# Kernel optimization log

Hardware: AMD Instinct MI355X
Metric: run time of the kernel (lower is better)

Reference implementation:

```python
import jax, jax.numpy as jnp
import numpy as np

B = 1024          # global batch
D = 512           # embedding_size
C = 100000        # num_classes (sum over 8 shards)
S = 64.0          # ArcFace scale
M = 0.5           # ArcFace additive angular margin
EPS = 1e-30


def setup_inputs() -> dict:
    key = jax.random.key(0)
    k1, k2, k3 = jax.random.split(key, 3)
    embeddings = jax.random.normal(k1, (B, D), dtype=jnp.float32)
    weight = jax.random.normal(k2, (C, D), dtype=jnp.float32)
    labels = jax.random.randint(k3, (B,), 0, C, dtype=jnp.int64)
    return {"embeddings": embeddings, "weight": weight, "labels": labels}


def reference(embeddings, weight, labels):
    # normalize(embeddings), normalize(weight) -> cosine logits
    ne = embeddings * jax.lax.rsqrt(jnp.sum(embeddings * embeddings, axis=1, keepdims=True))
    nw = weight * jax.lax.rsqrt(jnp.sum(weight * weight, axis=1, keepdims=True))
    logits = jnp.clip(jnp.einsum("bd,cd->bc", ne, nw), -1.0, 1.0)  # [B, C]

    rows = jnp.arange(B)
    target_logit = logits[rows, labels]
    # ArcFace: cos(theta + m), theta+m clipped to pi (insightface CombinedMarginLoss m2)
    theta = jnp.arccos(jnp.clip(target_logit, -1.0, 1.0))
    new_target = jnp.cos(jnp.minimum(theta + M, jnp.float32(np.pi)))
    logits = logits.at[rows, labels].set(new_target) * S

    # FusedDistCrossEntropy (single-device equivalent): stable softmax,
    # gather target prob, loss = -mean(log(clamp(p_target, 1e-30)))
    logp = jax.nn.log_softmax(logits, axis=1)
    p_target = jnp.exp(logp[rows, labels])
    loss = -jnp.mean(jnp.log(jnp.maximum(p_target, EPS)))
    return loss
```

## Files before the change

### kernel.cpp

```cpp
#include <hip/hip_runtime.h>
#include <hip/hip_bf16.h>
#include <math.h>
#include <stdint.h>

#define B_BATCH   1024
#define D_DIM     512
#define C_CLASSES 100000
#define BM        128
#define BN        128
#define BK        32
#define KITERS    (D_DIM / BK)
#define MTILES    (B_BATCH / BM)
#define NTILES    ((C_CLASSES + BN - 1) / BN)
#define LOG2E     1.44269504088896340736f
#define COSM      0.87758256189037276f
#define SINM      0.47942553860420301f
#define NEG_LOG_EPS 69.07755278982137f

typedef short bf16x8 __attribute__((ext_vector_type(8)));
typedef float f32x4  __attribute__((ext_vector_type(4)));

static __device__ __forceinline__ unsigned short f2bf(float f) {
    unsigned int u = __builtin_bit_cast(unsigned int, f);
    u += 0x7fffu + ((u >> 16) & 1u);
    return (unsigned short)(u >> 16);
}

static __device__ __forceinline__ void gld16(const unsigned short* g, unsigned short* l) {
    __builtin_amdgcn_global_load_lds(
        (const __attribute__((address_space(1))) unsigned int*)g,
        (__attribute__((address_space(3))) unsigned int*)l, 16, 0, 0);
}

__global__ __launch_bounds__(256) void norm_embed(const float* __restrict__ E,
                                                  unsigned short* __restrict__ Abf) {
    const int b = blockIdx.x;
    const int t = threadIdx.x;
    float2 v = ((const float2*)(E + (size_t)b * D_DIM))[t];
    float ss = v.x * v.x + v.y * v.y;
    #pragma unroll
    for (int off = 1; off < 64; off <<= 1) ss += __shfl_xor(ss, off);
    __shared__ float ws4[4];
    if ((t & 63) == 0) ws4[t >> 6] = ss;
    __syncthreads();
    float inv = rsqrtf(ws4[0] + ws4[1] + ws4[2] + ws4[3]);
    unsigned int packed = (unsigned int)f2bf(v.x * inv) |
                          ((unsigned int)f2bf(v.y * inv) << 16);
    ((unsigned int*)Abf)[(size_t)b * (D_DIM / 2) + t] = packed;
}

__global__ __launch_bounds__(256) void norm_weight(const float* __restrict__ W,
                                                   unsigned short* __restrict__ Wbf) {
    const int wave = threadIdx.x >> 6;
    const int lane = threadIdx.x & 63;
    const int row = blockIdx.x * 4 + wave;
    if (row >= C_CLASSES) return;
    const float4* src = (const float4*)(W + (size_t)row * D_DIM);
    float4 v0 = src[lane];
    float4 v1 = src[lane + 64];
    float ss = v0.x*v0.x + v0.y*v0.y + v0.z*v0.z + v0.w*v0.w
             + v1.x*v1.x + v1.y*v1.y + v1.z*v1.z + v1.w*v1.w;
    #pragma unroll
    for (int off = 1; off < 64; off <<= 1) ss += __shfl_xor(ss, off);
    float inv = rsqrtf(ss);
    ushort4 o0, o1;
    o0.x = f2bf(v0.x*inv); o0.y = f2bf(v0.y*inv); o0.z = f2bf(v0.z*inv); o0.w = f2bf(v0.w*inv);
    o1.x = f2bf(v1.x*inv); o1.y = f2bf(v1.y*inv); o1.z = f2bf(v1.z*inv); o1.w = f2bf(v1.w*inv);
    ushort4* dst = (ushort4*)(Wbf + (size_t)row * D_DIM);
    dst[lane] = o0;
    dst[lane + 64] = o1;
}

static __device__ __forceinline__ float epi_term(float accv, int col, int lab,
                                                 float* __restrict__ st, int srow) {
    float c = fminf(1.f, fmaxf(-1.f, accv));
    if (col >= C_CLASSES) return 0.f;
    float s = c * 64.0f;
    if (col == lab) {
        float sn = sqrtf(fmaxf(0.f, 1.f - c * c));
        float nm = c * COSM - sn * SINM;
        if (c < -COSM) nm = -1.f;
        s = nm * 64.0f;
        st[srow] = s;
    }
    return exp2f((s - 64.0f) * LOG2E);
}

__global__ __launch_bounds__(256) void gemm_cos(const unsigned short* __restrict__ Abf,
                                                const unsigned short* __restrict__ Wbf,
                                                const int* __restrict__ labels,
                                                float* __restrict__ st,
                                                float* __restrict__ partial) {
    __shared__ unsigned short As[BM * BK];
    __shared__ unsigned short Bs[BN * BK];
    __shared__ float rowSum[BM];
    __shared__ int   labs[BM];

    const int tid = threadIdx.x;
    const int m0 = blockIdx.x * BM;
    const int n0 = blockIdx.y * BN;
    if (tid < BM) { labs[tid] = labels[m0 + tid]; rowSum[tid] = 0.f; }

    const int lane = tid & 63;
    const int wave = tid >> 6;
    const int wm = wave & 1, wn = wave >> 1;
    const int l15 = lane & 15, quad = lane >> 4;

    const int rsub = lane >> 2;
    const int cg   = (lane & 3) * 8;
    const int c0 = wave * 2, c1 = wave * 2 + 1;
    const unsigned short* gA0 = Abf + (size_t)(m0 + c0 * 16 + rsub) * D_DIM + cg;
    const unsigned short* gA1 = Abf + (size_t)(m0 + c1 * 16 + rsub) * D_DIM + cg;
    const int bR0 = min(n0 + c0 * 16 + rsub, C_CLASSES - 1);
    const int bR1 = min(n0 + c1 * 16 + rsub, C_CLASSES - 1);
    const unsigned short* gB0 = Wbf + (size_t)bR0 * D_DIM + cg;
    const unsigned short* gB1 = Wbf + (size_t)bR1 * D_DIM + cg;
    unsigned short* lA0 = &As[c0 * 512];
    unsigned short* lA1 = &As[c1 * 512];
    unsigned short* lB0 = &Bs[c0 * 512];
    unsigned short* lB1 = &Bs[c1 * 512];

    const f32x4 z = (f32x4){0.f, 0.f, 0.f, 0.f};
    f32x4 a00 = z, a01 = z, a02 = z, a03 = z;
    f32x4 a10 = z, a11 = z, a12 = z, a13 = z;
    f32x4 a20 = z, a21 = z, a22 = z, a23 = z;
    f32x4 a30 = z, a31 = z, a32 = z, a33 = z;

    for (int kk = 0; kk < KITERS; ++kk) {
        __syncthreads();
        gld16(gA0, lA0); gld16(gA1, lA1);
        gld16(gB0, lB0); gld16(gB1, lB1);
        gA0 += BK; gA1 += BK; gB0 += BK; gB1 += BK;
        __syncthreads();

        const int aro = (wm * 64 + l15) * BK + quad * 8;
        const int bro = (wn * 64 + l15) * BK + quad * 8;
        bf16x8 af0 = *(const bf16x8*)&As[aro];
        bf16x8 af1 = *(const bf16x8*)&As[aro + 16 * BK];
        bf16x8 af2 = *(const bf16x8*)&As[aro + 32 * BK];
        bf16x8 af3 = *(const bf16x8*)&As[aro + 48 * BK];
        bf16x8 bf0 = *(const bf16x8*)&Bs[bro];
        bf16x8 bf1 = *(const bf16x8*)&Bs[bro + 16 * BK];
        bf16x8 bf2 = *(const bf16x8*)&Bs[bro + 32 * BK];
        bf16x8 bf3 = *(const bf16x8*)&Bs[bro + 48 * BK];

        a00 = __builtin_amdgcn_mfma_f32_16x16x32_bf16(af0, bf0, a00, 0, 0, 0);
        a01 = __builtin_amdgcn_mfma_f32_16x16x32_bf16(af0, bf1, a01, 0, 0, 0);
        a02 = __builtin_amdgcn_mfma_f32_16x16x32_bf16(af0, bf2, a02, 0, 0, 0);
        a03 = __builtin_amdgcn_mfma_f32_16x16x32_bf16(af0, bf3, a03, 0, 0, 0);
        a10 = __builtin_amdgcn_mfma_f32_16x16x32_bf16(af1, bf0, a10, 0, 0, 0);
        a11 = __builtin_amdgcn_mfma_f32_16x16x32_bf16(af1, bf1, a11, 0, 0, 0);
        a12 = __builtin_amdgcn_mfma_f32_16x16x32_bf16(af1, bf2, a12, 0, 0, 0);
        a13 = __builtin_amdgcn_mfma_f32_16x16x32_bf16(af1, bf3, a13, 0, 0, 0);
        a20 = __builtin_amdgcn_mfma_f32_16x16x32_bf16(af2, bf0, a20, 0, 0, 0);
        a21 = __builtin_amdgcn_mfma_f32_16x16x32_bf16(af2, bf1, a21, 0, 0, 0);
        a22 = __builtin_amdgcn_mfma_f32_16x16x32_bf16(af2, bf2, a22, 0, 0, 0);
        a23 = __builtin_amdgcn_mfma_f32_16x16x32_bf16(af2, bf3, a23, 0, 0, 0);
        a30 = __builtin_amdgcn_mfma_f32_16x16x32_bf16(af3, bf0, a30, 0, 0, 0);
        a31 = __builtin_amdgcn_mfma_f32_16x16x32_bf16(af3, bf1, a31, 0, 0, 0);
        a32 = __builtin_amdgcn_mfma_f32_16x16x32_bf16(af3, bf2, a32, 0, 0, 0);
        a33 = __builtin_amdgcn_mfma_f32_16x16x32_bf16(af3, bf3, a33, 0, 0, 0);
    }

    const int colbase = n0 + wn * 64 + l15;

    #define EPIROW(A0, A1, A2, A3, MI)                                         \
    {                                                                          \
        _Pragma("unroll")                                                      \
        for (int r = 0; r < 4; ++r) {                                          \
            const int rloc = wm * 64 + (MI) * 16 + quad * 4 + r;               \
            const int lab = labs[rloc];                                        \
            float part = 0.f;                                                  \
            part += epi_term((A0)[r], colbase,      lab, st, m0 + rloc);       \
            part += epi_term((A1)[r], colbase + 16, lab, st, m0 + rloc);       \
            part += epi_term((A2)[r], colbase + 32, lab, st, m0 + rloc);       \
            part += epi_term((A3)[r], colbase + 48, lab, st, m0 + rloc);       \
            part += __shfl_xor(part, 1);                                       \
            part += __shfl_xor(part, 2);                                       \
            part += __shfl_xor(part, 4);                                       \
            part += __shfl_xor(part, 8);                                       \
            if (l15 == 0) atomicAdd(&rowSum[rloc], part);                      \
        }                                                                      \
    }

    EPIROW(a00, a01, a02, a03, 0)
    EPIROW(a10, a11, a12, a13, 1)
    EPIROW(a20, a21, a22, a23, 2)
    EPIROW(a30, a31, a32, a33, 3)
    #undef EPIROW

    __syncthreads();
    if (tid < BM) partial[(size_t)blockIdx.y * B_BATCH + m0 + tid] = rowSum[tid];
}

__global__ __launch_bounds__(64) void reduce_loss(const float* __restrict__ partial,
                                                  const float* __restrict__ st,
                                                  float* __restrict__ out) {
    const int b = blockIdx.x * 64 + threadIdx.x;
    float L = 0.f;
    for (int t = 0; t < NTILES; ++t) L += partial[(size_t)t * B_BATCH + b];
    float logp = st[b] - 64.0f - logf(L);
    float lossb = fminf(-logp, NEG_LOG_EPS) * (1.0f / (float)B_BATCH);
    #pragma unroll
    for (int off = 1; off < 64; off <<= 1) lossb += __shfl_xor(lossb, off);
    if (threadIdx.x == 0) atomicAdd(out, lossb);
}

extern "C" void kernel_launch(void* const* d_in, const int* in_sizes, int n_in,
                              void* d_out, int out_size, void* d_ws, size_t ws_size,
                              hipStream_t stream) {
    const float* emb = (const float*)d_in[0];
    const float* wgt = (const float*)d_in[1];
    const int*   lab = (const int*)d_in[2];
    float* out = (float*)d_out;
    char* ws = (char*)d_ws;

    const size_t WBF_B = (size_t)C_CLASSES * D_DIM * 2;
    const size_t ABF_B = (size_t)B_BATCH * D_DIM * 2;

    unsigned short* Wbf = (unsigned short*)ws;
    unsigned short* Abf = (unsigned short*)(ws + WBF_B);
    float* st      = (float*)(ws + WBF_B + ABF_B);
    float* partial = (float*)(ws + WBF_B + ABF_B + 4096);

    hipMemsetAsync(d_out, 0, sizeof(float), stream);
    norm_embed<<<B_BATCH, 256, 0, stream>>>(emb, Abf);
    norm_weight<<<(C_CLASSES + 3) / 4, 256, 0, stream>>>(wgt, Wbf);
    gemm_cos<<<dim3(MTILES, NTILES), 256, 0, stream>>>(Abf, Wbf, lab, st, partial);
    reduce_loss<<<16, 64, 0, stream>>>(partial, st, out);
}
```

Baseline: 498.5 us.

## Double-buffer LDS tiles and remap block ids for L2 locality

```diff
diff --git a/kernel.cpp b/kernel.cpp
--- a/kernel.cpp
+++ b/kernel.cpp
@@ -12,6 +12,8 @@
 #define KITERS    (D_DIM / BK)
 #define MTILES    (B_BATCH / BM)
 #define NTILES    ((C_CLASSES + BN - 1) / BN)
+#define NGROUPS   98
+#define GRID_G    (8 * 8 * NGROUPS)
 #define LOG2E     1.44269504088896340736f
 #define COSM      0.87758256189037276f
 #define SINM      0.47942553860420301f
@@ -91,14 +93,21 @@
                                                 const int* __restrict__ labels,
                                                 float* __restrict__ st,
                                                 float* __restrict__ partial) {
-    __shared__ unsigned short As[BM * BK];
-    __shared__ unsigned short Bs[BN * BK];
+    __shared__ unsigned short As[2][BM * BK];
+    __shared__ unsigned short Bs[2][BN * BK];
     __shared__ float rowSum[BM];
     __shared__ int   labs[BM];
 
+    const int id = blockIdx.x;
+    const int x  = id & 7;
+    const int s  = id >> 3;
+    const int mt = s & 7;
+    const int y  = x + 8 * (s >> 3);
+    if (y >= NTILES) return;
+    const int m0 = mt * BM;
+    const int n0 = y * BN;
+
     const int tid = threadIdx.x;
-    const int m0 = blockIdx.x * BM;
-    const int n0 = blockIdx.y * BN;
     if (tid < BM) { labs[tid] = labels[m0 + tid]; rowSum[tid] = 0.f; }
 
     const int lane = tid & 63;
@@ -115,10 +124,7 @@
     const int bR1 = min(n0 + c1 * 16 + rsub, C_CLASSES - 1);
     const unsigned short* gB0 = Wbf + (size_t)bR0 * D_DIM + cg;
     const unsigned short* gB1 = Wbf + (size_t)bR1 * D_DIM + cg;
-    unsigned short* lA0 = &As[c0 * 512];
-    unsigned short* lA1 = &As[c1 * 512];
-    unsigned short* lB0 = &Bs[c0 * 512];
-    unsigned short* lB1 = &Bs[c1 * 512];
+    const int lo0 = c0 * 512, lo1 = c1 * 512;
 
     const f32x4 z = (f32x4){0.f, 0.f, 0.f, 0.f};
     f32x4 a00 = z, a01 = z, a02 = z, a03 = z;
@@ -126,23 +132,31 @@
     f32x4 a20 = z, a21 = z, a22 = z, a23 = z;
     f32x4 a30 = z, a31 = z, a32 = z, a33 = z;
 
+    const int aro = (wm * 64 + l15) * BK + quad * 8;
+    const int bro = (wn * 64 + l15) * BK + quad * 8;
+
+    gld16(gA0, &As[0][lo0]); gld16(gA1, &As[0][lo1]);
+    gld16(gB0, &Bs[0][lo0]); gld16(gB1, &Bs[0][lo1]);
+    gA0 += BK; gA1 += BK; gB0 += BK; gB1 += BK;
+
+    #pragma unroll
     for (int kk = 0; kk < KITERS; ++kk) {
+        const int cur = kk & 1, nxt = cur ^ 1;
         __syncthreads();
-        gld16(gA0, lA0); gld16(gA1, lA1);
-        gld16(gB0, lB0); gld16(gB1, lB1);
-        gA0 += BK; gA1 += BK; gB0 += BK; gB1 += BK;
-        __syncthreads();
-
-        const int aro = (wm * 64 + l15) * BK + quad * 8;
-        const int bro = (wn * 64 + l15) * BK + quad * 8;
-        bf16x8 af0 = *(const bf16x8*)&As[aro];
-        bf16x8 af1 = *(const bf16x8*)&As[aro + 16 * BK];
-        bf16x8 af2 = *(const bf16x8*)&As[aro + 32 * BK];
-        bf16x8 af3 = *(const bf16x8*)&As[aro + 48 * BK];
-        bf16x8 bf0 = *(const bf16x8*)&Bs[bro];
-        bf16x8 bf1 = *(const bf16x8*)&Bs[bro + 16 * BK];
-        bf16x8 bf2 = *(const bf16x8*)&Bs[bro + 32 * BK];
-        bf16x8 bf3 = *(const bf16x8*)&Bs[bro + 48 * BK];
+        if (kk + 1 < KITERS) {
+            gld16(gA0, &As[nxt][lo0]); gld16(gA1, &As[nxt][lo1]);
+            gld16(gB0, &Bs[nxt][lo0]); gld16(gB1, &Bs[nxt][lo1]);
+            gA0 += BK; gA1 += BK; gB0 += BK; gB1 += BK;
+        }
+
+        bf16x8 af0 = *(const bf16x8*)&As[cur][aro];
+        bf16x8 af1 = *(const bf16x8*)&As[cur][aro + 16 * BK];
+        bf16x8 af2 = *(const bf16x8*)&As[cur][aro + 32 * BK];
+        bf16x8 af3 = *(const bf16x8*)&As[cur][aro + 48 * BK];
+        bf16x8 bf0 = *(const bf16x8*)&Bs[cur][bro];
+        bf16x8 bf1 = *(const bf16x8*)&Bs[cur][bro + 16 * BK];
+        bf16x8 bf2 = *(const bf16x8*)&Bs[cur][bro + 32 * BK];
+        bf16x8 bf3 = *(const bf16x8*)&Bs[cur][bro + 48 * BK];
 
         a00 = __builtin_amdgcn_mfma_f32_16x16x32_bf16(af0, bf0, a00, 0, 0, 0);
         a01 = __builtin_amdgcn_mfma_f32_16x16x32_bf16(af0, bf1, a01, 0, 0, 0);
@@ -190,7 +204,7 @@
     #undef EPIROW
 
     __syncthreads();
-    if (tid < BM) partial[(size_t)blockIdx.y * B_BATCH + m0 + tid] = rowSum[tid];
+    if (tid < BM) partial[(size_t)y * B_BATCH + m0 + tid] = rowSum[tid];
 }
 
 __global__ __launch_bounds__(64) void reduce_loss(const float* __restrict__ partial,
@@ -226,6 +240,6 @@
     hipMemsetAsync(d_out, 0, sizeof(float), stream);
     norm_embed<<<B_BATCH, 256, 0, stream>>>(emb, Abf);
     norm_weight<<<(C_CLASSES + 3) / 4, 256, 0, stream>>>(wgt, Wbf);
-    gemm_cos<<<dim3(MTILES, NTILES), 256, 0, stream>>>(Abf, Wbf, lab, st, partial);
+    gemm_cos<<<GRID_G, 256, 0, stream>>>(Abf, Wbf, lab, st, partial);
     reduce_loss<<<16, 64, 0, stream>>>(partial, st, out);
 }
```

Measured after the change: 554.9 us. +11.3%, slower.
